# Kernel tuning notes

Hardware: AMD Instinct MI355X
Metric: run time of the kernel (lower is better)

The kernel has to match this reference:

```python
import jax, jax.numpy as jnp
import numpy as np

N, E, D, H = 50000, 600000, 128, 8
C = D // H  # per-head channels

def _layernorm(x, g, b, eps=1e-5):
    mu = jnp.mean(x, axis=-1, keepdims=True)
    var = jnp.var(x, axis=-1, keepdims=True)
    return (x - mu) * jax.lax.rsqrt(var + eps) * g + b

def setup_inputs() -> dict:
    key = jax.random.key(0)
    ks = jax.random.split(key, 16)
    s = 0.02
    w = lambda k, shape: jax.random.normal(k, shape, jnp.float32) * s
    return {
        "x": jax.random.normal(ks[0], (N, D), jnp.float32),
        "edge_attr": jax.random.normal(ks[1], (E, D), jnp.float32),
        "edge_index": jax.random.randint(ks[2], (2, E), 0, N, jnp.int64),
        # TransformerConv params (PyG: lin_query/key/value with bias, lin_edge no bias, lin_skip root weight)
        "Wq": w(ks[3], (D, D)), "bq": jnp.zeros((D,), jnp.float32),
        "Wk": w(ks[4], (D, D)), "bk": jnp.zeros((D,), jnp.float32),
        "Wv": w(ks[5], (D, D)), "bv": jnp.zeros((D,), jnp.float32),
        "We": w(ks[6], (D, D)),
        "Wskip": w(ks[7], (D, D)), "bskip": jnp.zeros((D,), jnp.float32),
        # FFN
        "W1": w(ks[8], (D, 4 * D)), "b1": jnp.zeros((4 * D,), jnp.float32),
        "W2": w(ks[9], (4 * D, D)), "b2": jnp.zeros((D,), jnp.float32),
        # LayerNorms + residual scale
        "g1": jnp.ones((D,), jnp.float32), "beta1": jnp.zeros((D,), jnp.float32),
        "g2": jnp.ones((D,), jnp.float32), "beta2": jnp.zeros((D,), jnp.float32),
        "alpha": jnp.ones((1,), jnp.float32),
    }

def reference(x, edge_attr, edge_index, Wq, bq, Wk, bk, Wv, bv, We, Wskip, bskip,
              W1, b1, W2, b2, g1, beta1, g2, beta2, alpha):
    n = x.shape[0]
    src, dst = edge_index[0], edge_index[1]

    h = _layernorm(x, g1, beta1)

    # --- TransformerConv ---
    q = (h @ Wq + bq)[dst].reshape(-1, H, C)              # [E,H,C]
    e = (edge_attr @ We).reshape(-1, H, C)                # [E,H,C]
    k = (h @ Wk + bk)[src].reshape(-1, H, C) + e          # [E,H,C]
    v = (h @ Wv + bv)[src].reshape(-1, H, C) + e          # [E,H,C]

    logits = jnp.sum(q * k, axis=-1) / jnp.sqrt(jnp.float32(C))  # [E,H]
    # segment softmax over incoming edges per destination node
    m = jax.ops.segment_max(logits, dst, num_segments=n)          # [N,H]
    p = jnp.exp(logits - m[dst])                                   # [E,H]
    z = jax.ops.segment_sum(p, dst, num_segments=n)               # [N,H]
    attn = p / (z[dst] + 1e-16)                                    # [E,H]

    msg = attn[..., None] * v                                      # [E,H,C]
    out = jax.ops.segment_sum(msg, dst, num_segments=n).reshape(n, H * C)
    out = out + h @ Wskip + bskip                                  # root weight (skip)

    x = x + alpha * out

    h2 = _layernorm(x, g2, beta2)
    ffn = jax.nn.silu(h2 @ W1 + b1) @ W2 + b2
    return x + ffn
```

## Files before the change

### kernel.cpp

```cpp
#include <hip/hip_runtime.h>
#include <hip/hip_bf16.h>

typedef __bf16 bf16x8 __attribute__((ext_vector_type(8)));
typedef __bf16 bf16x4 __attribute__((ext_vector_type(4)));
typedef __bf16 bf16x2 __attribute__((ext_vector_type(2)));
typedef float f32x4 __attribute__((ext_vector_type(4)));
using bf16 = __hip_bfloat16;

__global__ __launch_bounds__(256) void t_k(const float* __restrict__ W,
                                           bf16* __restrict__ WT, int K, int N)
{
    int idx = blockIdx.x * 256 + threadIdx.x;
    if (idx >= K * N) return;
    int n = idx / K, k = idx % K;
    WT[idx] = __float2bfloat16(W[(size_t)k * N + n]);
}

__global__ __launch_bounds__(256) void bcat_k(const float* __restrict__ a, const float* __restrict__ b,
                                              const float* __restrict__ c, const float* __restrict__ d,
                                              float* __restrict__ o)
{
    int i = threadIdx.x + blockIdx.x * 256;
    if (i >= 512) return;
    o[i] = (i < 128) ? a[i] : (i < 256) ? b[i - 128] : (i < 384) ? c[i - 256] : d[i - 384];
}

template <int MODE, bool AF32>
__global__ __launch_bounds__(512) void gemm2_k(
    const void* __restrict__ Av, const bf16* __restrict__ WT,
    const float* __restrict__ bias, void* __restrict__ Cout,
    const float* __restrict__ resid, const int* __restrict__ rowperm,
    int M, int K, int Nout)
{
    __shared__ __bf16 As[128 * 128];
    __shared__ __bf16 Ws[128 * 128];

    const int tid  = threadIdx.x;
    const int wave = tid >> 6;
    const int lane = tid & 63;
    const int row0 = blockIdx.x * 128;
    const int col0 = blockIdx.y * 128;

    f32x4 acc[8];
#pragma unroll
    for (int i = 0; i < 8; i++) acc[i] = (f32x4){0.f, 0.f, 0.f, 0.f};

    for (int k0 = 0; k0 < K; k0 += 128) {
        if constexpr (AF32) {
            const float* A = (const float*)Av;
#pragma unroll
            for (int i = 0; i < 8; i++) {
                int idx = tid + i * 512;
                int r = idx >> 5, c4 = idx & 31;
                bf16x4 o;
                if (row0 + r < M) {
                    f32x4 v = *reinterpret_cast<const f32x4*>(A + (size_t)(row0 + r) * K + k0 + c4 * 4);
#pragma unroll
                    for (int j = 0; j < 4; j++) o[j] = (__bf16)v[j];
                } else {
#pragma unroll
                    for (int j = 0; j < 4; j++) o[j] = (__bf16)0.f;
                }
                int col = (c4 >> 1) ^ (r & 7);
                *reinterpret_cast<bf16x4*>(&As[r * 128 + col * 8 + (c4 & 1) * 4]) = o;
            }
        } else {
            const bf16* A = (const bf16*)Av;
#pragma unroll
            for (int i = 0; i < 4; i++) {
                int idx = tid + i * 512;
                int r = idx >> 4, c = idx & 15;
                bf16x8 v;
                if (row0 + r < M) {
                    v = *reinterpret_cast<const bf16x8*>(A + (size_t)(row0 + r) * K + k0 + c * 8);
                } else {
#pragma unroll
                    for (int j = 0; j < 8; j++) v[j] = (__bf16)0.f;
                }
                *reinterpret_cast<bf16x8*>(&As[r * 128 + ((c ^ (r & 7)) * 8)]) = v;
            }
        }
#pragma unroll
        for (int i = 0; i < 4; i++) {
            int idx = tid + i * 512;
            int r = idx >> 4, c = idx & 15;
            bf16x8 v = *reinterpret_cast<const bf16x8*>(WT + (size_t)(col0 + r) * K + k0 + c * 8);
            *reinterpret_cast<bf16x8*>(&Ws[r * 128 + ((c ^ (r & 7)) * 8)]) = v;
        }
        __syncthreads();

        const int mrow = wave * 16 + (lane & 15);
        const int kq = lane >> 4;
#pragma unroll
        for (int kk = 0; kk < 4; kk++) {
            int cidx = kk * 4 + kq;
            bf16x8 a = *reinterpret_cast<const bf16x8*>(&As[mrow * 128 + ((cidx ^ (mrow & 7)) * 8)]);
#pragma unroll
            for (int ct = 0; ct < 8; ct++) {
                int nrow = ct * 16 + (lane & 15);
                bf16x8 b = *reinterpret_cast<const bf16x8*>(&Ws[nrow * 128 + ((cidx ^ (nrow & 7)) * 8)]);
                acc[ct] = __builtin_amdgcn_mfma_f32_16x16x32_bf16(a, b, acc[ct], 0, 0, 0);
            }
        }
        __syncthreads();
    }

    const int rbase = row0 + wave * 16 + ((lane >> 4) << 2);
    int orow[4];
#pragma unroll
    for (int r = 0; r < 4; r++) {
        int row = rbase + r;
        orow[r] = (row < M) ? (rowperm ? rowperm[row] : row) : -1;
    }
#pragma unroll
    for (int ct = 0; ct < 8; ct++) {
        int col = col0 + ct * 16 + (lane & 15);
        float bv = bias ? bias[col] : 0.f;
#pragma unroll
        for (int r = 0; r < 4; r++) {
            if (orow[r] < 0) continue;
            float v = acc[ct][r] + bv;
            if constexpr (MODE == 2) v = v / (1.f + __expf(-v));
            if constexpr (MODE == 3) v += resid[(size_t)orow[r] * 128 + col];
            if constexpr (MODE == 3) {
                ((float*)Cout)[(size_t)orow[r] * Nout + col] = v;
            } else {
                ((bf16*)Cout)[(size_t)orow[r] * Nout + col] = __float2bfloat16(v);
            }
        }
    }
}

__global__ __launch_bounds__(256) void egemm_k(
    const float* __restrict__ A, const bf16* __restrict__ WT,
    bf16* __restrict__ C, const int* __restrict__ rowperm, int M)
{
    __shared__ __bf16 Ws[128 * 128];
#pragma unroll
    for (int i = 0; i < 8; i++) {
        int idx = threadIdx.x + i * 256;
        int r = idx >> 4, c = idx & 15;
        bf16x8 v = *reinterpret_cast<const bf16x8*>(WT + r * 128 + c * 8);
        *reinterpret_cast<bf16x8*>(&Ws[r * 128 + ((c ^ (r & 7)) * 8)]) = v;
    }
    __syncthreads();

    const int lane = threadIdx.x & 63;
    const int wave = threadIdx.x >> 6;
    const int r16  = lane & 15;
    const int kq   = lane >> 4;
    const int ntiles = (M + 15) >> 4;

    for (int t = blockIdx.x * 4 + wave; t < ntiles; t += gridDim.x * 4) {
        const int row0 = t * 16;
        const int arow = row0 + r16;

        bf16x8 a[4];
        if (arow < M) {
            const float* ap = A + (size_t)arow * 128 + kq * 8;
#pragma unroll
            for (int kk = 0; kk < 4; kk++) {
                f32x4 lo = *reinterpret_cast<const f32x4*>(ap + kk * 32);
                f32x4 hi = *reinterpret_cast<const f32x4*>(ap + kk * 32 + 4);
#pragma unroll
                for (int j = 0; j < 4; j++) {
                    a[kk][j]     = (__bf16)lo[j];
                    a[kk][j + 4] = (__bf16)hi[j];
                }
            }
        } else {
#pragma unroll
            for (int kk = 0; kk < 4; kk++)
#pragma unroll
                for (int j = 0; j < 8; j++) a[kk][j] = (__bf16)0.f;
        }

        f32x4 acc[8];
#pragma unroll
        for (int i = 0; i < 8; i++) acc[i] = (f32x4){0.f, 0.f, 0.f, 0.f};
#pragma unroll
        for (int kk = 0; kk < 4; kk++) {
            int cidx = kk * 4 + kq;
#pragma unroll
            for (int ct = 0; ct < 8; ct++) {
                int nrow = ct * 16 + r16;
                bf16x8 b = *reinterpret_cast<const bf16x8*>(&Ws[nrow * 128 + ((cidx ^ (nrow & 7)) * 8)]);
                acc[ct] = __builtin_amdgcn_mfma_f32_16x16x32_bf16(a[kk], b, acc[ct], 0, 0, 0);
            }
        }

        const int rbase = row0 + (kq << 2);
#pragma unroll
        for (int r = 0; r < 4; r++) {
            int row = rbase + r;
            if (row >= M) continue;
            size_t orow = (size_t)(rowperm ? rowperm[row] : row);
#pragma unroll
            for (int ct = 0; ct < 8; ct++) {
                C[orow * 128 + ct * 16 + r16] = __float2bfloat16(acc[ct][r]);
            }
        }
    }
}

template <int MODE>
__global__ __launch_bounds__(256) void ngemm_k(
    const bf16* __restrict__ A, const bf16* __restrict__ WT,
    const float* __restrict__ bias, bf16* __restrict__ C,
    int M, int Nout)
{
    __shared__ __bf16 Ws[128 * 128];
    const int col0 = blockIdx.y * 128;
#pragma unroll
    for (int i = 0; i < 8; i++) {
        int idx = threadIdx.x + i * 256;
        int r = idx >> 4, c = idx & 15;
        bf16x8 v = *reinterpret_cast<const bf16x8*>(WT + (size_t)(col0 + r) * 128 + c * 8);
        *reinterpret_cast<bf16x8*>(&Ws[r * 128 + ((c ^ (r & 7)) * 8)]) = v;
    }
    __syncthreads();

    const int lane = threadIdx.x & 63;
    const int wave = threadIdx.x >> 6;
    const int r16  = lane & 15;
    const int kq   = lane >> 4;
    const int ntiles = (M + 15) >> 4;

    float bcol[8];
#pragma unroll
    for (int ct = 0; ct < 8; ct++) bcol[ct] = bias[col0 + ct * 16 + r16];

    for (int t = blockIdx.x * 4 + wave; t < ntiles; t += gridDim.x * 4) {
        const int row0 = t * 16;
        const int arow = row0 + r16;

        bf16x8 a[4];
        if (arow < M) {
            const bf16* ap = A + (size_t)arow * 128 + kq * 8;
#pragma unroll
            for (int kk = 0; kk < 4; kk++)
                a[kk] = *reinterpret_cast<const bf16x8*>(ap + kk * 32);
        } else {
#pragma unroll
            for (int kk = 0; kk < 4; kk++)
#pragma unroll
                for (int j = 0; j < 8; j++) a[kk][j] = (__bf16)0.f;
        }

        f32x4 acc[8];
#pragma unroll
        for (int i = 0; i < 8; i++) acc[i] = (f32x4){0.f, 0.f, 0.f, 0.f};
#pragma unroll
        for (int kk = 0; kk < 4; kk++) {
            int cidx = kk * 4 + kq;
#pragma unroll
            for (int ct = 0; ct < 8; ct++) {
                int nrow = ct * 16 + r16;
                bf16x8 b = *reinterpret_cast<const bf16x8*>(&Ws[nrow * 128 + ((cidx ^ (nrow & 7)) * 8)]);
                acc[ct] = __builtin_amdgcn_mfma_f32_16x16x32_bf16(a[kk], b, acc[ct], 0, 0, 0);
            }
        }

        const int rbase = row0 + (kq << 2);
#pragma unroll
        for (int r = 0; r < 4; r++) {
            int row = rbase + r;
            if (row >= M) continue;
#pragma unroll
            for (int ct = 0; ct < 8; ct++) {
                float v = acc[ct][r] + bcol[ct];
                if constexpr (MODE == 2) v = v / (1.f + __expf(-v));
                C[(size_t)row * Nout + col0 + ct * 16 + r16] = __float2bfloat16(v);
            }
        }
    }
}

__global__ __launch_bounds__(256) void ln_k(
    const float* __restrict__ x, const float* __restrict__ g,
    const float* __restrict__ beta, bf16* __restrict__ h, int Nrows)
{
    int row = blockIdx.x * 4 + (threadIdx.x >> 6);
    int lane = threadIdx.x & 63;
    if (row >= Nrows) return;
    size_t base = (size_t)row * 128;
    float v0 = x[base + lane], v1 = x[base + lane + 64];
    float s = v0 + v1, ss = v0 * v0 + v1 * v1;
#pragma unroll
    for (int off = 32; off; off >>= 1) {
        s += __shfl_xor(s, off, 64);
        ss += __shfl_xor(ss, off, 64);
    }
    float mu = s * (1.f / 128.f);
    float var = ss * (1.f / 128.f) - mu * mu;
    float rs = rsqrtf(var + 1e-5f);
    h[base + lane]      = __float2bfloat16((v0 - mu) * rs * g[lane] + beta[lane]);
    h[base + lane + 64] = __float2bfloat16((v1 - mu) * rs * g[lane + 64] + beta[lane + 64]);
}

__global__ __launch_bounds__(256) void hist_k(const int* __restrict__ ei, int* __restrict__ cnt, int E)
{
    int e = blockIdx.x * 256 + threadIdx.x;
    if (e < E) atomicAdd(&cnt[ei[E + e]], 1);
}

__global__ __launch_bounds__(1024) void scan_k(const int* __restrict__ cnt, int* __restrict__ offset, int N)
{
    __shared__ int wsum[16];
    __shared__ int s_running;
    int tid  = threadIdx.x;
    int lane = tid & 63;
    int wv   = tid >> 6;
    if (tid == 0) { s_running = 0; offset[0] = 0; }
    __syncthreads();
    for (int base = 0; base < N; base += 1024) {
        int v = (base + tid < N) ? cnt[base + tid] : 0;
        int s = v;
#pragma unroll
        for (int d = 1; d < 64; d <<= 1) {
            int t = __shfl_up(s, d, 64);
            if (lane >= d) s += t;
        }
        if (lane == 63) wsum[wv] = s;
        __syncthreads();
        if (tid == 0) {
            int acc = 0;
#pragma unroll
            for (int i = 0; i < 16; i++) { acc += wsum[i]; wsum[i] = acc; }
        }
        __syncthreads();
        int run = s_running;
        int wexcl = (wv > 0) ? wsum[wv - 1] : 0;
        if (base + tid < N) offset[base + tid + 1] = run + wexcl + s;
        __syncthreads();
        if (tid == 0) s_running = run + wsum[15];
        __syncthreads();
    }
}

__global__ __launch_bounds__(256) void scatter_k(
    const int* __restrict__ ei, const int* __restrict__ offset,
    int* __restrict__ cursor, int* __restrict__ srcs, int* __restrict__ epos, int E)
{
    int e = blockIdx.x * 256 + threadIdx.x;
    if (e >= E) return;
    int src = ei[e];
    int dst = ei[E + e];
    int r = atomicAdd(&cursor[dst], 1);
    int j = offset[dst] + r;
    srcs[j] = src;
    epos[e] = j;
}

__global__ __launch_bounds__(256) void gather_k(
    const int* __restrict__ srcs, const int* __restrict__ offset,
    const bf16* __restrict__ QKVS, const bf16* __restrict__ Ep,
    const float* __restrict__ x, const float* __restrict__ alpha,
    const float* __restrict__ g, const float* __restrict__ beta,
    float* __restrict__ xn, bf16* __restrict__ h2, int N)
{
    int node = blockIdx.x * 4 + (threadIdx.x >> 6);
    if (node >= N) return;
    int lane = threadIdx.x & 63;
    int c = lane * 2;

    bf16x2 qv = *reinterpret_cast<const bf16x2*>(QKVS + (size_t)node * 512 + c);
    float q0 = (float)qv[0], q1 = (float)qv[1];

    int start = offset[node], end = offset[node + 1];
    float den = 0.f, num0 = 0.f, num1 = 0.f;

    bf16x2 kv, vv, ev;
    if (start < end) {
        const bf16* sp = QKVS + (size_t)srcs[start] * 512 + c;
        kv = *reinterpret_cast<const bf16x2*>(sp + 128);
        vv = *reinterpret_cast<const bf16x2*>(sp + 256);
        ev = *reinterpret_cast<const bf16x2*>(Ep + (size_t)start * 128 + c);
    }
    for (int j = start; j < end; j++) {
        bf16x2 kc = kv, vc = vv, ec = ev;
        if (j + 1 < end) {
            const bf16* sp = QKVS + (size_t)srcs[j + 1] * 512 + c;
            kv = *reinterpret_cast<const bf16x2*>(sp + 128);
            vv = *reinterpret_cast<const bf16x2*>(sp + 256);
            ev = *reinterpret_cast<const bf16x2*>(Ep + (size_t)(j + 1) * 128 + c);
        }
        float e0 = (float)ec[0], e1 = (float)ec[1];
        float part = q0 * ((float)kc[0] + e0) + q1 * ((float)kc[1] + e1);
        part += __shfl_xor(part, 1, 64);
        part += __shfl_xor(part, 2, 64);
        part += __shfl_xor(part, 4, 64);
        float p = __expf(part * 0.25f);
        den  += p;
        num0 += p * ((float)vc[0] + e0);
        num1 += p * ((float)vc[1] + e1);
    }

    size_t base = (size_t)node * 128;
    float invz = 1.f / (den + 1e-16f);
    float al = alpha[0];
    float s0 = (float)QKVS[(size_t)node * 512 + 384 + c];
    float s1 = (float)QKVS[(size_t)node * 512 + 384 + c + 1];
    float o0 = num0 * invz + s0;
    float o1 = num1 * invz + s1;
    float x0 = x[base + c] + al * o0;
    float x1 = x[base + c + 1] + al * o1;
    xn[base + c] = x0;
    xn[base + c + 1] = x1;

    float s = x0 + x1, ss = x0 * x0 + x1 * x1;
#pragma unroll
    for (int off = 32; off; off >>= 1) {
        s += __shfl_xor(s, off, 64);
        ss += __shfl_xor(ss, off, 64);
    }
    float mu = s * (1.f / 128.f);
    float var = ss * (1.f / 128.f) - mu * mu;
    float rs = rsqrtf(var + 1e-5f);
    h2[base + c]     = __float2bfloat16((x0 - mu) * rs * g[c] + beta[c]);
    h2[base + c + 1] = __float2bfloat16((x1 - mu) * rs * g[c + 1] + beta[c + 1]);
}

extern "C" void kernel_launch(void* const* d_in, const int* in_sizes, int n_in,
                              void* d_out, int out_size, void* d_ws, size_t ws_size,
                              hipStream_t stream)
{
    const float* x         = (const float*)d_in[0];
    const float* edge_attr = (const float*)d_in[1];
    const int*   ei        = (const int*)d_in[2];
    const float* Wq = (const float*)d_in[3];  const float* bq = (const float*)d_in[4];
    const float* Wk = (const float*)d_in[5];  const float* bk = (const float*)d_in[6];
    const float* Wv = (const float*)d_in[7];  const float* bv = (const float*)d_in[8];
    const float* We = (const float*)d_in[9];
    const float* Wskip = (const float*)d_in[10]; const float* bskip = (const float*)d_in[11];
    const float* W1 = (const float*)d_in[12]; const float* b1 = (const float*)d_in[13];
    const float* W2 = (const float*)d_in[14]; const float* b2 = (const float*)d_in[15];
    const float* g1 = (const float*)d_in[16]; const float* beta1 = (const float*)d_in[17];
    const float* g2 = (const float*)d_in[18]; const float* beta2 = (const float*)d_in[19];
    const float* alpha = (const float*)d_in[20];

    const int N = in_sizes[0] / 128;
    const int E = in_sizes[2] / 2;

    char* w = (char*)d_ws;
    auto alloc = [&](size_t bytes) {
        char* p = w;
        w += (bytes + 255) & ~(size_t)255;
        return p;
    };
    bf16*  h      = (bf16*)alloc((size_t)N * 128 * 2);
    bf16*  QKVS   = (bf16*)alloc((size_t)N * 512 * 2);
    bf16*  Ep     = (bf16*)alloc((size_t)E * 128 * 2);
    float* xn     = (float*)alloc((size_t)N * 128 * 4);
    bf16*  h2     = (bf16*)alloc((size_t)N * 128 * 2);
    bf16*  t      = (bf16*)alloc((size_t)N * 512 * 2);
    int*   cnt    = (int*)alloc((size_t)N * 4);
    int*   cursor = (int*)alloc((size_t)N * 4);
    int*   offset = (int*)alloc((size_t)(N + 1) * 4);
    int*   srcs   = (int*)alloc((size_t)E * 4);
    int*   epos   = (int*)alloc((size_t)E * 4);
    bf16*  WTqkvs = (bf16*)alloc((size_t)512 * 128 * 2);
    bf16*  WTe    = (bf16*)alloc((size_t)128 * 128 * 2);
    bf16*  WT1    = (bf16*)alloc((size_t)512 * 128 * 2);
    bf16*  WT2    = (bf16*)alloc((size_t)128 * 512 * 2);
    float* bqkvs  = (float*)alloc((size_t)512 * 4);

    t_k<<<64, 256, 0, stream>>>(Wq, WTqkvs, 128, 128);
    t_k<<<64, 256, 0, stream>>>(Wk, WTqkvs + 128 * 128, 128, 128);
    t_k<<<64, 256, 0, stream>>>(Wv, WTqkvs + 256 * 128, 128, 128);
    t_k<<<64, 256, 0, stream>>>(Wskip, WTqkvs + 384 * 128, 128, 128);
    t_k<<<64, 256, 0, stream>>>(We, WTe, 128, 128);
    t_k<<<256, 256, 0, stream>>>(W1, WT1, 128, 512);
    t_k<<<256, 256, 0, stream>>>(W2, WT2, 512, 128);
    bcat_k<<<2, 256, 0, stream>>>(bq, bk, bv, bskip, bqkvs);

    hipMemsetAsync(cnt, 0, (size_t)N * 4, stream);
    hipMemsetAsync(cursor, 0, (size_t)N * 4, stream);
    hist_k<<<(E + 255) / 256, 256, 0, stream>>>(ei, cnt, E);
    scan_k<<<1, 1024, 0, stream>>>(cnt, offset, N);
    scatter_k<<<(E + 255) / 256, 256, 0, stream>>>(ei, offset, cursor, srcs, epos, E);

    ln_k<<<(N + 3) / 4, 256, 0, stream>>>(x, g1, beta1, h, N);

    ngemm_k<0><<<dim3(256, 4), 256, 0, stream>>>(h, WTqkvs, bqkvs, QKVS, N, 512);

    egemm_k<<<1280, 256, 0, stream>>>(edge_attr, WTe, Ep, epos, E);

    gather_k<<<(N + 3) / 4, 256, 0, stream>>>(srcs, offset, QKVS, Ep, x, alpha, g2, beta2, xn, h2, N);

    ngemm_k<2><<<dim3(256, 4), 256, 0, stream>>>(h2, WT1, b1, t, N, 512);
    gemm2_k<3, false><<<dim3((N + 127) / 128, 1), 512, 0, stream>>>(t, WT2, b2, d_out, xn, nullptr, N, 512, 128);
}
```

Baseline: 824.2 us.

## Merge weight prep launches and replace FFN down-proj with persistent weight-stationary GEMM

Folds seven weight transpose launches and the bias concat into one prep kernel, and merges the two memsets into a single memset spanning cnt and cursor. The final FFN down-projection changes from a 128x128-tiled GEMM that re-streams weights every K step to a persistent kernel. That kernel keeps a 64x512 weight slice in LDS and loops over 16-row tiles, holding the full K row of A in registers. This cuts launch overhead and weight reloads. It relies on cursor being allocated directly after cnt, and the 64 KB LDS footprint and large register usage may limit occupancy.

```diff
diff --git a/kernel.cpp b/kernel.cpp
--- a/kernel.cpp
+++ b/kernel.cpp
@@ -7,127 +7,35 @@
 typedef float f32x4 __attribute__((ext_vector_type(4)));
 using bf16 = __hip_bfloat16;
 
-__global__ __launch_bounds__(256) void t_k(const float* __restrict__ W,
-                                           bf16* __restrict__ WT, int K, int N)
+__global__ __launch_bounds__(256) void prep_k(
+    const float* __restrict__ Wq, const float* __restrict__ Wk,
+    const float* __restrict__ Wv, const float* __restrict__ Wskip,
+    const float* __restrict__ We, const float* __restrict__ W1,
+    const float* __restrict__ W2,
+    const float* __restrict__ bq, const float* __restrict__ bk,
+    const float* __restrict__ bv, const float* __restrict__ bskip,
+    bf16* __restrict__ WTqkvs, bf16* __restrict__ WTe,
+    bf16* __restrict__ WT1, bf16* __restrict__ WT2, float* __restrict__ bqkvs)
 {
     int idx = blockIdx.x * 256 + threadIdx.x;
-    if (idx >= K * N) return;
-    int n = idx / K, k = idx % K;
-    WT[idx] = __float2bfloat16(W[(size_t)k * N + n]);
-}
-
-__global__ __launch_bounds__(256) void bcat_k(const float* __restrict__ a, const float* __restrict__ b,
-                                              const float* __restrict__ c, const float* __restrict__ d,
-                                              float* __restrict__ o)
-{
-    int i = threadIdx.x + blockIdx.x * 256;
-    if (i >= 512) return;
-    o[i] = (i < 128) ? a[i] : (i < 256) ? b[i - 128] : (i < 384) ? c[i - 256] : d[i - 384];
-}
-
-template <int MODE, bool AF32>
-__global__ __launch_bounds__(512) void gemm2_k(
-    const void* __restrict__ Av, const bf16* __restrict__ WT,
-    const float* __restrict__ bias, void* __restrict__ Cout,
-    const float* __restrict__ resid, const int* __restrict__ rowperm,
-    int M, int K, int Nout)
-{
-    __shared__ __bf16 As[128 * 128];
-    __shared__ __bf16 Ws[128 * 128];
-
-    const int tid  = threadIdx.x;
-    const int wave = tid >> 6;
-    const int lane = tid & 63;
-    const int row0 = blockIdx.x * 128;
-    const int col0 = blockIdx.y * 128;
-
-    f32x4 acc[8];
-#pragma unroll
-    for (int i = 0; i < 8; i++) acc[i] = (f32x4){0.f, 0.f, 0.f, 0.f};
-
-    for (int k0 = 0; k0 < K; k0 += 128) {
-        if constexpr (AF32) {
-            const float* A = (const float*)Av;
-#pragma unroll
-            for (int i = 0; i < 8; i++) {
-                int idx = tid + i * 512;
-                int r = idx >> 5, c4 = idx & 31;
-                bf16x4 o;
-                if (row0 + r < M) {
-                    f32x4 v = *reinterpret_cast<const f32x4*>(A + (size_t)(row0 + r) * K + k0 + c4 * 4);
-#pragma unroll
-                    for (int j = 0; j < 4; j++) o[j] = (__bf16)v[j];
-                } else {
-#pragma unroll
-                    for (int j = 0; j < 4; j++) o[j] = (__bf16)0.f;
-                }
-                int col = (c4 >> 1) ^ (r & 7);
-                *reinterpret_cast<bf16x4*>(&As[r * 128 + col * 8 + (c4 & 1) * 4]) = o;
-            }
-        } else {
-            const bf16* A = (const bf16*)Av;
-#pragma unroll
-            for (int i = 0; i < 4; i++) {
-                int idx = tid + i * 512;
-                int r = idx >> 4, c = idx & 15;
-                bf16x8 v;
-                if (row0 + r < M) {
-                    v = *reinterpret_cast<const bf16x8*>(A + (size_t)(row0 + r) * K + k0 + c * 8);
-                } else {
-#pragma unroll
-                    for (int j = 0; j < 8; j++) v[j] = (__bf16)0.f;
-                }
-                *reinterpret_cast<bf16x8*>(&As[r * 128 + ((c ^ (r & 7)) * 8)]) = v;
-            }
-        }
-#pragma unroll
-        for (int i = 0; i < 4; i++) {
-            int idx = tid + i * 512;
-            int r = idx >> 4, c = idx & 15;
-            bf16x8 v = *reinterpret_cast<const bf16x8*>(WT + (size_t)(col0 + r) * K + k0 + c * 8);
-            *reinterpret_cast<bf16x8*>(&Ws[r * 128 + ((c ^ (r & 7)) * 8)]) = v;
-        }
-        __syncthreads();
-
-        const int mrow = wave * 16 + (lane & 15);
-        const int kq = lane >> 4;
-#pragma unroll
-        for (int kk = 0; kk < 4; kk++) {
-            int cidx = kk * 4 + kq;
-            bf16x8 a = *reinterpret_cast<const bf16x8*>(&As[mrow * 128 + ((cidx ^ (mrow & 7)) * 8)]);
-#pragma unroll
-            for (int ct = 0; ct < 8; ct++) {
-                int nrow = ct * 16 + (lane & 15);
-                bf16x8 b = *reinterpret_cast<const bf16x8*>(&Ws[nrow * 128 + ((cidx ^ (nrow & 7)) * 8)]);
-                acc[ct] = __builtin_amdgcn_mfma_f32_16x16x32_bf16(a, b, acc[ct], 0, 0, 0);
-            }
-        }
-        __syncthreads();
-    }
-
-    const int rbase = row0 + wave * 16 + ((lane >> 4) << 2);
-    int orow[4];
-#pragma unroll
-    for (int r = 0; r < 4; r++) {
-        int row = rbase + r;
-        orow[r] = (row < M) ? (rowperm ? rowperm[row] : row) : -1;
-    }
-#pragma unroll
-    for (int ct = 0; ct < 8; ct++) {
-        int col = col0 + ct * 16 + (lane & 15);
-        float bv = bias ? bias[col] : 0.f;
-#pragma unroll
-        for (int r = 0; r < 4; r++) {
-            if (orow[r] < 0) continue;
-            float v = acc[ct][r] + bv;
-            if constexpr (MODE == 2) v = v / (1.f + __expf(-v));
-            if constexpr (MODE == 3) v += resid[(size_t)orow[r] * 128 + col];
-            if constexpr (MODE == 3) {
-                ((float*)Cout)[(size_t)orow[r] * Nout + col] = v;
-            } else {
-                ((bf16*)Cout)[(size_t)orow[r] * Nout + col] = __float2bfloat16(v);
-            }
-        }
+    if (idx < 81920) {
+        int w = idx >> 14;
+        int i = idx & 16383;
+        int n = i >> 7, k = i & 127;
+        const float* src = (w == 0) ? Wq : (w == 1) ? Wk : (w == 2) ? Wv : (w == 3) ? Wskip : We;
+        bf16* dst = (w < 4) ? (WTqkvs + (w << 14)) : WTe;
+        dst[i] = __float2bfloat16(src[k * 128 + n]);
+    } else if (idx < 81920 + 65536) {
+        int i = idx - 81920;
+        int n = i >> 7, k = i & 127;
+        WT1[i] = __float2bfloat16(W1[k * 512 + n]);
+    } else if (idx < 81920 + 131072) {
+        int i = idx - 81920 - 65536;
+        int n = i >> 9, k = i & 511;
+        WT2[i] = __float2bfloat16(W2[k * 128 + n]);
+    } else if (idx < 81920 + 131072 + 512) {
+        int i = idx - 81920 - 131072;
+        bqkvs[i] = (i < 128) ? bq[i] : (i < 256) ? bk[i - 128] : (i < 384) ? bv[i - 256] : bskip[i - 384];
     }
 }
 
@@ -271,6 +179,77 @@
                 float v = acc[ct][r] + bcol[ct];
                 if constexpr (MODE == 2) v = v / (1.f + __expf(-v));
                 C[(size_t)row * Nout + col0 + ct * 16 + r16] = __float2bfloat16(v);
+            }
+        }
+    }
+}
+
+__global__ __launch_bounds__(512) void ngemm64_k(
+    const bf16* __restrict__ A, const bf16* __restrict__ WT,
+    const float* __restrict__ bias, const float* __restrict__ resid,
+    float* __restrict__ Cout, int M)
+{
+    __shared__ __bf16 Ws[64 * 512];
+    const int col0 = blockIdx.y * 64;
+#pragma unroll
+    for (int i = 0; i < 8; i++) {
+        int idx = threadIdx.x + i * 512;
+        int r = idx >> 6, c = idx & 63;
+        bf16x8 v = *reinterpret_cast<const bf16x8*>(WT + (size_t)(col0 + r) * 512 + c * 8);
+        *reinterpret_cast<bf16x8*>(&Ws[r * 512 + ((c ^ (r & 7)) * 8)]) = v;
+    }
+    __syncthreads();
+
+    const int lane = threadIdx.x & 63;
+    const int wave = threadIdx.x >> 6;
+    const int r16  = lane & 15;
+    const int kq   = lane >> 4;
+    const int ntiles = (M + 15) >> 4;
+
+    float bcol[4];
+#pragma unroll
+    for (int ct = 0; ct < 4; ct++) bcol[ct] = bias[col0 + ct * 16 + r16];
+
+    for (int t = blockIdx.x * 8 + wave; t < ntiles; t += gridDim.x * 8) {
+        const int row0 = t * 16;
+        const int arow = row0 + r16;
+
+        bf16x8 a[16];
+        if (arow < M) {
+            const bf16* ap = A + (size_t)arow * 512 + kq * 8;
+#pragma unroll
+            for (int kk = 0; kk < 16; kk++)
+                a[kk] = *reinterpret_cast<const bf16x8*>(ap + kk * 32);
+        } else {
+#pragma unroll
+            for (int kk = 0; kk < 16; kk++)
+#pragma unroll
+                for (int j = 0; j < 8; j++) a[kk][j] = (__bf16)0.f;
+        }
+
+        f32x4 acc[4];
+#pragma unroll
+        for (int i = 0; i < 4; i++) acc[i] = (f32x4){0.f, 0.f, 0.f, 0.f};
+#pragma unroll
+        for (int kk = 0; kk < 16; kk++) {
+            int cidx = kk * 4 + kq;
+#pragma unroll
+            for (int ct = 0; ct < 4; ct++) {
+                int nrow = ct * 16 + r16;
+                bf16x8 b = *reinterpret_cast<const bf16x8*>(&Ws[nrow * 512 + ((cidx ^ (nrow & 7)) * 8)]);
+                acc[ct] = __builtin_amdgcn_mfma_f32_16x16x32_bf16(a[kk], b, acc[ct], 0, 0, 0);
+            }
+        }
+
+        const int rbase = row0 + (kq << 2);
+#pragma unroll
+        for (int r = 0; r < 4; r++) {
+            int row = rbase + r;
+            if (row >= M) continue;
+#pragma unroll
+            for (int ct = 0; ct < 4; ct++) {
+                int col = col0 + ct * 16 + r16;
+                Cout[(size_t)row * 128 + col] = acc[ct][r] + bcol[ct] + resid[(size_t)row * 128 + col];
             }
         }
     }
@@ -465,17 +444,11 @@
     bf16*  WT2    = (bf16*)alloc((size_t)128 * 512 * 2);
     float* bqkvs  = (float*)alloc((size_t)512 * 4);
 
-    t_k<<<64, 256, 0, stream>>>(Wq, WTqkvs, 128, 128);
-    t_k<<<64, 256, 0, stream>>>(Wk, WTqkvs + 128 * 128, 128, 128);
-    t_k<<<64, 256, 0, stream>>>(Wv, WTqkvs + 256 * 128, 128, 128);
-    t_k<<<64, 256, 0, stream>>>(Wskip, WTqkvs + 384 * 128, 128, 128);
-    t_k<<<64, 256, 0, stream>>>(We, WTe, 128, 128);
-    t_k<<<256, 256, 0, stream>>>(W1, WT1, 128, 512);
-    t_k<<<256, 256, 0, stream>>>(W2, WT2, 512, 128);
-    bcat_k<<<2, 256, 0, stream>>>(bq, bk, bv, bskip, bqkvs);
-
-    hipMemsetAsync(cnt, 0, (size_t)N * 4, stream);
-    hipMemsetAsync(cursor, 0, (size_t)N * 4, stream);
+    prep_k<<<834, 256, 0, stream>>>(Wq, Wk, Wv, Wskip, We, W1, W2,
+                                    bq, bk, bv, bskip,
+                                    WTqkvs, WTe, WT1, WT2, bqkvs);
+
+    hipMemsetAsync(cnt, 0, (size_t)((char*)cursor - (char*)cnt) + (size_t)N * 4, stream);
     hist_k<<<(E + 255) / 256, 256, 0, stream>>>(ei, cnt, E);
     scan_k<<<1, 1024, 0, stream>>>(cnt, offset, N);
     scatter_k<<<(E + 255) / 256, 256, 0, stream>>>(ei, offset, cursor, srcs, epos, E);
@@ -489,5 +462,5 @@
     gather_k<<<(N + 3) / 4, 256, 0, stream>>>(srcs, offset, QKVS, Ep, x, alpha, g2, beta2, xn, h2, N);
 
     ngemm_k<2><<<dim3(256, 4), 256, 0, stream>>>(h2, WT1, b1, t, N, 512);
-    gemm2_k<3, false><<<dim3((N + 127) / 128, 1), 512, 0, stream>>>(t, WT2, b2, d_out, xn, nullptr, N, 512, 128);
-}
+    ngemm64_k<<<dim3(256, 2), 512, 0, stream>>>(t, WT2, b2, xn, (float*)d_out, N);
+}
```

Measured after the change: 865.1 us. 5.0% more time.
